# Kernel optimization log

Hardware: AMD Instinct MI355X
Metric: run time of the kernel (lower is better)

The kernel has to match this reference:

```python
import jax, jax.numpy as jnp
import numpy as np

N_SEG, N_REG, N_EDGE, HID, CHEB_K = 40000, 1000, 640000, 256, 5


def setup_inputs() -> dict:
    key = jax.random.key(0)
    ks = jax.random.split(key, 6)
    return {
        "projected_region_features": jax.random.normal(ks[0], (N_REG, HID), jnp.float32),
        "segment2region_assignment": jax.random.uniform(ks[1], (N_SEG, N_REG), jnp.float32),
        "edge_index": jax.random.randint(ks[2], (2, N_EDGE), 0, N_SEG, dtype=jnp.int64),
        # ChebConv params: one [HID,HID] weight per Chebyshev order + shared bias
        "cheb_W": jax.random.normal(ks[3], (CHEB_K, HID, HID), jnp.float32) / np.sqrt(HID).astype(np.float32),
        "cheb_b": jnp.zeros((HID,), jnp.float32),
        "ln_gamma": jnp.ones((HID,), jnp.float32),
        "ln_beta": jnp.zeros((HID,), jnp.float32),
    }


def _cheb_conv(x, edge_index, W, b):
    """PyG ChebConv with normalization='sym', lambda_max=2.0.
    Scaled Laplacian L_hat = 2L/lam - I = -D^{-1/2} A D^{-1/2} (diag = 0)."""
    N = x.shape[0]
    src, dst = edge_index[0], edge_index[1]
    w = (src != dst).astype(x.dtype)  # remove_self_loops
    deg = jax.ops.segment_sum(w, src, num_segments=N)
    dinv = jnp.where(deg > 0, jax.lax.rsqrt(jnp.where(deg > 0, deg, 1.0)), 0.0)
    norm = -w * dinv[src] * dinv[dst]  # per-edge weight of L_hat

    def prop(t):  # y_i = sum_{(j->i)} norm_e * t_j
        return jax.ops.segment_sum(norm[:, None] * t[src], dst, num_segments=N)

    Tx0 = x
    out = Tx0 @ W[0]
    Tx1 = prop(Tx0)
    out = out + Tx1 @ W[1]
    for k in range(2, W.shape[0]):
        Tx2 = 2.0 * prop(Tx1) - Tx0
        out = out + Tx2 @ W[k]
        Tx0, Tx1 = Tx1, Tx2
    return out + b


def _layer_norm(x, g, b, eps=1e-5):
    mu = jnp.mean(x, axis=-1, keepdims=True)
    var = jnp.mean(jnp.square(x - mu), axis=-1, keepdims=True)
    return (x - mu) * jax.lax.rsqrt(var + eps) * g + b


def reference(projected_region_features, segment2region_assignment, edge_index,
              cheb_W, cheb_b, ln_gamma, ln_beta):
    # [n_seg, n_reg] @ [n_reg, hid] -> [n_seg, hid]
    seg_low_raw = segment2region_assignment @ projected_region_features
    seg_low = _cheb_conv(seg_low_raw, edge_index, cheb_W, cheb_b)
    seg_low = _layer_norm(jax.nn.gelu(seg_low, approximate=False), ln_gamma, ln_beta)
    return (seg_low, seg_low_raw)
```

## Files before the change

kernel.cpp:

```cpp
#include <hip/hip_runtime.h>

#define NSEG 40000
#define NREG 1000
#define NEDGE 640000
#define HID 256
#define KCAT 1280
#define LPAD 40
#define NBLK 157

typedef float f32x4 __attribute__((ext_vector_type(4)));
typedef short s16x8 __attribute__((ext_vector_type(8)));
typedef unsigned short u16x4 __attribute__((ext_vector_type(4)));
typedef unsigned short u16x8 __attribute__((ext_vector_type(8)));

__device__ __forceinline__ unsigned short f2bf(float f) {
    unsigned u = __builtin_bit_cast(unsigned, f);
    u += 0x7FFFu + ((u >> 16) & 1u);
    return (unsigned short)(u >> 16);
}
__device__ __forceinline__ float bf2f(unsigned short h) {
    unsigned u = ((unsigned)h) << 16;
    return __builtin_bit_cast(float, u);
}

__global__ void detect_kernel(const unsigned int* __restrict__ E, int* flag) {
    int lane = threadIdx.x;
    unsigned v = E[2 * lane + 1];
    unsigned long long m = __ballot(v == 0u);
    if (lane == 0) *flag = (__popcll(m) >= 48) ? 1 : 0;
}

__device__ __forceinline__ int edge_at(const void* E, int idx, int is64) {
    return is64 ? (int)((const long long*)E)[idx] : ((const int*)E)[idx];
}

__global__ __launch_bounds__(256) void deg_cnt_kernel(const void* __restrict__ E,
                                                      const int* __restrict__ flag,
                                                      int* deg, int* cnt) {
    int e = blockIdx.x * 256 + threadIdx.x;
    if (e >= NEDGE) return;
    int is64 = *flag;
    int s = edge_at(E, e, is64);
    int d = edge_at(E, e + NEDGE, is64);
    if (s != d) {
        atomicAdd(&deg[s], 1);
        atomicAdd(&cnt[d], 1);
    }
}

__global__ __launch_bounds__(256) void dinv_kernel(const int* __restrict__ deg,
                                                   float* __restrict__ dinv) {
    int i = blockIdx.x * 256 + threadIdx.x;
    if (i < NSEG) {
        int d = deg[i];
        dinv[i] = d > 0 ? rsqrtf((float)d) : 0.f;
    }
}

__global__ __launch_bounds__(256) void scan1_kernel(const int* __restrict__ cnt,
                                                    int* __restrict__ bsum) {
    __shared__ int sh[256];
    int t = threadIdx.x;
    int i = blockIdx.x * 256 + t;
    sh[t] = (i < NSEG) ? cnt[i] : 0;
    __syncthreads();
    for (int o = 128; o > 0; o >>= 1) {
        if (t < o) sh[t] += sh[t + o];
        __syncthreads();
    }
    if (t == 0) bsum[blockIdx.x] = sh[0];
}

__global__ __launch_bounds__(256) void scan2_kernel(const int* __restrict__ bsum,
                                                    int* __restrict__ boff,
                                                    int* __restrict__ rowptr) {
    __shared__ int sh[256];
    int t = threadIdx.x;
    int v = (t < NBLK) ? bsum[t] : 0;
    sh[t] = v;
    __syncthreads();
    for (int o = 1; o < 256; o <<= 1) {
        int x = 0;
        if (t >= o) x = sh[t - o];
        __syncthreads();
        if (t >= o) sh[t] += x;
        __syncthreads();
    }
    if (t < NBLK) boff[t] = sh[t] - v;
    if (t == 255) rowptr[NSEG] = sh[255];
}

__global__ __launch_bounds__(256) void scan3_kernel(const int* __restrict__ cnt,
                                                    const int* __restrict__ boff,
                                                    int* __restrict__ rowptr,
                                                    int* __restrict__ cursor) {
    __shared__ int sh[256];
    int t = threadIdx.x;
    int i = blockIdx.x * 256 + t;
    int v = (i < NSEG) ? cnt[i] : 0;
    sh[t] = v;
    __syncthreads();
    for (int o = 1; o < 256; o <<= 1) {
        int x = 0;
        if (t >= o) x = sh[t - o];
        __syncthreads();
        if (t >= o) sh[t] += x;
        __syncthreads();
    }
    if (i < NSEG) {
        int p = boff[blockIdx.x] + sh[t] - v;
        rowptr[i] = p;
        cursor[i] = p;
    }
}

__global__ __launch_bounds__(256) void scatter_kernel(const void* __restrict__ E,
                                                      const int* __restrict__ flag,
                                                      const float* __restrict__ dinv,
                                                      int* cursor,
                                                      int* __restrict__ colidx,
                                                      float* __restrict__ val) {
    int e = blockIdx.x * 256 + threadIdx.x;
    if (e >= NEDGE) return;
    int is64 = *flag;
    int s = edge_at(E, e, is64);
    int d = edge_at(E, e + NEDGE, is64);
    if (s != d) {
        int pos = atomicAdd(&cursor[d], 1);
        colidx[pos] = s;
        val[pos] = -dinv[s] * dinv[d];
    }
}

__global__ void prep_pt_kernel(const float* __restrict__ P, unsigned short* __restrict__ Pt) {
    int n = blockIdx.x;
    for (int k = threadIdx.x; k < NREG; k += blockDim.x)
        Pt[(size_t)n * NREG + k] = f2bf(P[(size_t)k * HID + n]);
}
__global__ void prep_wt_kernel(const float* __restrict__ W, unsigned short* __restrict__ Wt) {
    int n = blockIdx.x;
    for (int k = threadIdx.x; k < KCAT; k += blockDim.x)
        Wt[(size_t)n * KCAT + k] = f2bf(W[(size_t)k * HID + n]);
}

__global__ __launch_bounds__(256) void gemm1_kernel(const float* __restrict__ S,
                                                    const unsigned short* __restrict__ Pt,
                                                    float* __restrict__ raw,
                                                    unsigned short* __restrict__ xcat) {
    __shared__ unsigned short As[64][LPAD];
    __shared__ unsigned short Bs[256][LPAD];
    const int m0 = blockIdx.x * 64;
    const int tid = threadIdx.x;
    const int lane = tid & 63, wn = tid >> 6;
    const int r = lane & 15, q = lane >> 4;
    const int srow = tid >> 2, scol = (tid & 3) * 8;

    f32x4 acc[4][4] = {};

    for (int kb = 0; kb < NREG; kb += 32) {
        const bool kvalid = (kb + scol + 8 <= NREG);
        u16x8 av = {0, 0, 0, 0, 0, 0, 0, 0};
        u16x8 bv0 = av, bv1 = av, bv2 = av, bv3 = av;
        if (kvalid) {
            const float* sp = S + (size_t)(m0 + srow) * NREG + kb + scol;
            f32x4 f0 = *(const f32x4*)sp;
            f32x4 f1 = *(const f32x4*)(sp + 4);
            av[0] = f2bf(f0[0]); av[1] = f2bf(f0[1]); av[2] = f2bf(f0[2]); av[3] = f2bf(f0[3]);
            av[4] = f2bf(f1[0]); av[5] = f2bf(f1[1]); av[6] = f2bf(f1[2]); av[7] = f2bf(f1[3]);
            bv0 = *(const u16x8*)(Pt + (size_t)(srow)       * NREG + kb + scol);
            bv1 = *(const u16x8*)(Pt + (size_t)(srow +  64) * NREG + kb + scol);
            bv2 = *(const u16x8*)(Pt + (size_t)(srow + 128) * NREG + kb + scol);
            bv3 = *(const u16x8*)(Pt + (size_t)(srow + 192) * NREG + kb + scol);
        }
        __syncthreads();
        *(u16x8*)&As[srow][scol] = av;
        *(u16x8*)&Bs[srow][scol] = bv0;
        *(u16x8*)&Bs[srow + 64][scol] = bv1;
        *(u16x8*)&Bs[srow + 128][scol] = bv2;
        *(u16x8*)&Bs[srow + 192][scol] = bv3;
        __syncthreads();
        s16x8 af[4], bfv[4];
#pragma unroll
        for (int am = 0; am < 4; ++am) af[am] = *(const s16x8*)&As[am * 16 + r][q * 8];
#pragma unroll
        for (int bn = 0; bn < 4; ++bn) bfv[bn] = *(const s16x8*)&Bs[wn * 64 + bn * 16 + r][q * 8];
#pragma unroll
        for (int am = 0; am < 4; ++am) {
#pragma unroll
            for (int bn = 0; bn < 4; ++bn)
                acc[am][bn] = __builtin_amdgcn_mfma_f32_16x16x32_bf16(af[am], bfv[bn], acc[am][bn], 0, 0, 0);
        }
    }
#pragma unroll
    for (int am = 0; am < 4; ++am) {
        int rowb = m0 + am * 16 + q * 4;
#pragma unroll
        for (int bn = 0; bn < 4; ++bn) {
            int col = wn * 64 + bn * 16 + r;
#pragma unroll
            for (int i = 0; i < 4; ++i) {
                float v = acc[am][bn][i];
                raw[(size_t)(rowb + i) * HID + col] = v;
                xcat[(size_t)(rowb + i) * KCAT + col] = f2bf(v);
            }
        }
    }
}

__global__ __launch_bounds__(256) void prop_kernel(unsigned short* xcat,
                                                   const int* __restrict__ rowptr,
                                                   const int* __restrict__ colidx,
                                                   const float* __restrict__ val,
                                                   int inOff, int outOff, int subOff,
                                                   float scale) {
    int g = blockIdx.x * 4 + (threadIdx.x >> 6);
    int lane = threadIdx.x & 63;
    int e0 = rowptr[g], e1 = rowptr[g + 1];
    float a0 = 0.f, a1 = 0.f, a2 = 0.f, a3 = 0.f;
    const unsigned short* xin = xcat + inOff + lane * 4;
    for (int base = e0; base < e1; base += 64) {
        int m = e1 - base;
        if (m > 64) m = 64;
        int cc = 0;
        float vv = 0.f;
        if (lane < m) {
            cc = colidx[base + lane];
            vv = val[base + lane];
        }
        int i = 0;
        for (; i + 8 <= m; i += 8) {
            u16x4 t[8];
#pragma unroll
            for (int j = 0; j < 8; ++j) {
                int c = __shfl(cc, i + j);
                t[j] = *(const u16x4*)(xin + (size_t)c * KCAT);
            }
#pragma unroll
            for (int j = 0; j < 8; ++j) {
                float v = __shfl(vv, i + j);
                a0 += v * bf2f(t[j][0]);
                a1 += v * bf2f(t[j][1]);
                a2 += v * bf2f(t[j][2]);
                a3 += v * bf2f(t[j][3]);
            }
        }
        for (; i < m; ++i) {
            int c = __shfl(cc, i);
            float v = __shfl(vv, i);
            u16x4 t = *(const u16x4*)(xin + (size_t)c * KCAT);
            a0 += v * bf2f(t[0]);
            a1 += v * bf2f(t[1]);
            a2 += v * bf2f(t[2]);
            a3 += v * bf2f(t[3]);
        }
    }
    a0 *= scale; a1 *= scale; a2 *= scale; a3 *= scale;
    if (subOff >= 0) {
        u16x4 p = *(const u16x4*)(xcat + (size_t)g * KCAT + subOff + lane * 4);
        a0 -= bf2f(p[0]); a1 -= bf2f(p[1]); a2 -= bf2f(p[2]); a3 -= bf2f(p[3]);
    }
    u16x4 o = {f2bf(a0), f2bf(a1), f2bf(a2), f2bf(a3)};
    *(u16x4*)(xcat + (size_t)g * KCAT + outOff + lane * 4) = o;
}

__global__ __launch_bounds__(256) void gemm2_kernel(const unsigned short* __restrict__ xcat,
                                                    const unsigned short* __restrict__ Wt,
                                                    const float* __restrict__ bias,
                                                    const float* __restrict__ gamma,
                                                    const float* __restrict__ beta,
                                                    float* __restrict__ outp) {
    __shared__ unsigned short As[64][LPAD];
    __shared__ unsigned short Bs[256][LPAD];
    __shared__ float rs[64][4];
    __shared__ float rss[64][4];
    const int m0 = blockIdx.x * 64;
    const int tid = threadIdx.x;
    const int lane = tid & 63, wn = tid >> 6;
    const int r = lane & 15, q = lane >> 4;
    const int srow = tid >> 2, scol = (tid & 3) * 8;

    f32x4 acc[4][4] = {};

    for (int kb = 0; kb < KCAT; kb += 32) {
        u16x8 av  = *(const u16x8*)(xcat + (size_t)(m0 + srow) * KCAT + kb + scol);
        u16x8 bv0 = *(const u16x8*)(Wt + (size_t)(srow)       * KCAT + kb + scol);
        u16x8 bv1 = *(const u16x8*)(Wt + (size_t)(srow +  64) * KCAT + kb + scol);
        u16x8 bv2 = *(const u16x8*)(Wt + (size_t)(srow + 128) * KCAT + kb + scol);
        u16x8 bv3 = *(const u16x8*)(Wt + (size_t)(srow + 192) * KCAT + kb + scol);
        __syncthreads();
        *(u16x8*)&As[srow][scol] = av;
        *(u16x8*)&Bs[srow][scol] = bv0;
        *(u16x8*)&Bs[srow + 64][scol] = bv1;
        *(u16x8*)&Bs[srow + 128][scol] = bv2;
        *(u16x8*)&Bs[srow + 192][scol] = bv3;
        __syncthreads();
        s16x8 af[4], bfv[4];
#pragma unroll
        for (int am = 0; am < 4; ++am) af[am] = *(const s16x8*)&As[am * 16 + r][q * 8];
#pragma unroll
        for (int bn = 0; bn < 4; ++bn) bfv[bn] = *(const s16x8*)&Bs[wn * 64 + bn * 16 + r][q * 8];
#pragma unroll
        for (int am = 0; am < 4; ++am) {
#pragma unroll
            for (int bn = 0; bn < 4; ++bn)
                acc[am][bn] = __builtin_amdgcn_mfma_f32_16x16x32_bf16(af[am], bfv[bn], acc[am][bn], 0, 0, 0);
        }
    }

    float bc[4], gm[4], bt[4];
#pragma unroll
    for (int bn = 0; bn < 4; ++bn) {
        int col = wn * 64 + bn * 16 + r;
        bc[bn] = bias[col];
        gm[bn] = gamma[col];
        bt[bn] = beta[col];
    }
#pragma unroll
    for (int am = 0; am < 4; ++am) {
#pragma unroll
        for (int i = 0; i < 4; ++i) {
            float s = 0.f, ss = 0.f;
#pragma unroll
            for (int bn = 0; bn < 4; ++bn) {
                float v = acc[am][bn][i] + bc[bn];
                v = 0.5f * v * (1.f + erff(v * 0.70710678118654752f));
                acc[am][bn][i] = v;
                s += v;
                ss += v * v;
            }
#pragma unroll
            for (int msk = 1; msk < 16; msk <<= 1) {
                s += __shfl_xor(s, msk);
                ss += __shfl_xor(ss, msk);
            }
            if (r == 0) {
                int row = am * 16 + q * 4 + i;
                rs[row][wn] = s;
                rss[row][wn] = ss;
            }
        }
    }
    __syncthreads();
#pragma unroll
    for (int am = 0; am < 4; ++am) {
#pragma unroll
        for (int i = 0; i < 4; ++i) {
            int row = am * 16 + q * 4 + i;
            float s = rs[row][0] + rs[row][1] + rs[row][2] + rs[row][3];
            float ss = rss[row][0] + rss[row][1] + rss[row][2] + rss[row][3];
            float mu = s * (1.f / HID);
            float var = ss * (1.f / HID) - mu * mu;
            float inv = rsqrtf(var + 1e-5f);
#pragma unroll
            for (int bn = 0; bn < 4; ++bn) {
                int col = wn * 64 + bn * 16 + r;
                outp[(size_t)(m0 + row) * HID + col] = (acc[am][bn][i] - mu) * inv * gm[bn] + bt[bn];
            }
        }
    }
}

extern "C" void kernel_launch(void* const* d_in, const int* in_sizes, int n_in,
                              void* d_out, int out_size, void* d_ws, size_t ws_size,
                              hipStream_t stream) {
    const float* P     = (const float*)d_in[0];
    const float* S     = (const float*)d_in[1];
    const void*  E     = d_in[2];
    const float* W     = (const float*)d_in[3];
    const float* bias  = (const float*)d_in[4];
    const float* gamma = (const float*)d_in[5];
    const float* beta  = (const float*)d_in[6];

    float* out = (float*)d_out;
    float* raw = out + (size_t)NSEG * HID;

    char* ws = (char*)d_ws;
    size_t off = 0;
    auto alloc = [&](size_t bytes) -> void* {
        void* p = ws + off;
        off += (bytes + 255) & ~(size_t)255;
        return p;
    };
    unsigned short* xcat   = (unsigned short*)alloc((size_t)NSEG * KCAT * 2);
    unsigned short* Pt     = (unsigned short*)alloc((size_t)HID * NREG * 2);
    unsigned short* Wt     = (unsigned short*)alloc((size_t)HID * KCAT * 2);
    int*            deg    = (int*)alloc((size_t)NSEG * 4);
    float*          dinv   = (float*)alloc((size_t)NSEG * 4);
    int*            cnt    = (int*)alloc((size_t)NSEG * 4);
    int*            rowptr = (int*)alloc((size_t)(NSEG + 1) * 4);
    int*            cursor = (int*)alloc((size_t)NSEG * 4);
    int*            colidx = (int*)alloc((size_t)NEDGE * 4);
    float*          val    = (float*)alloc((size_t)NEDGE * 4);
    int*            bsum   = (int*)alloc((size_t)NBLK * 4);
    int*            boff   = (int*)alloc((size_t)NBLK * 4);
    int*            flag   = (int*)alloc(256);
    if (off > ws_size) return;

    hipMemsetAsync(deg, 0, (size_t)NSEG * 4, stream);
    hipMemsetAsync(cnt, 0, (size_t)NSEG * 4, stream);

    detect_kernel<<<1, 64, 0, stream>>>((const unsigned int*)E, flag);
    prep_pt_kernel<<<HID, 256, 0, stream>>>(P, Pt);
    prep_wt_kernel<<<HID, 256, 0, stream>>>(W, Wt);

    deg_cnt_kernel<<<NEDGE / 256, 256, 0, stream>>>(E, flag, deg, cnt);
    dinv_kernel<<<(NSEG + 255) / 256, 256, 0, stream>>>(deg, dinv);
    scan1_kernel<<<NBLK, 256, 0, stream>>>(cnt, bsum);
    scan2_kernel<<<1, 256, 0, stream>>>(bsum, boff, rowptr);
    scan3_kernel<<<NBLK, 256, 0, stream>>>(cnt, boff, rowptr, cursor);
    scatter_kernel<<<NEDGE / 256, 256, 0, stream>>>(E, flag, dinv, cursor, colidx, val);

    gemm1_kernel<<<NSEG / 64, 256, 0, stream>>>(S, Pt, raw, xcat);

    prop_kernel<<<NSEG / 4, 256, 0, stream>>>(xcat, rowptr, colidx, val, 0 * HID, 1 * HID, -1, 1.f);
    prop_kernel<<<NSEG / 4, 256, 0, stream>>>(xcat, rowptr, colidx, val, 1 * HID, 2 * HID, 0 * HID, 2.f);
    prop_kernel<<<NSEG / 4, 256, 0, stream>>>(xcat, rowptr, colidx, val, 2 * HID, 3 * HID, 1 * HID, 2.f);
    prop_kernel<<<NSEG / 4, 256, 0, stream>>>(xcat, rowptr, colidx, val, 3 * HID, 4 * HID, 2 * HID, 2.f);

    gemm2_kernel<<<NSEG / 64, 256, 0, stream>>>(xcat, Wt, bias, gamma, beta, out);
}
```

Before: 469.7 us.

## Double-buffer GEMMs with direct global-to-LDS loads and 512-thread blocks

Both GEMM kernels are rewritten to double-buffer LDS tiles, using global_load_lds DMA for the bf16 operands with an XOR-swizzled layout in place of padded rows. Blocks grow to 8 waves laid out as a 2x4 grid, so each wave holds fewer accumulators. Pt is padded to K=1024 with zeros so the tail tile needs no bounds check. The aim is to overlap memory fetch with MFMA work and drop one barrier per k-step. The cost is more LDS per block and tighter coupling to the swizzle and DMA lane mapping.

New measurement: 445.1 us. 5.2% less time.

```diff
diff --git a/kernel.cpp b/kernel.cpp
--- a/kernel.cpp
+++ b/kernel.cpp
@@ -5,7 +5,7 @@
 #define NEDGE 640000
 #define HID 256
 #define KCAT 1280
-#define LPAD 40
+#define KP1 1024
 #define NBLK 157
 
 typedef float f32x4 __attribute__((ext_vector_type(4)));
@@ -13,6 +13,13 @@
 typedef unsigned short u16x4 __attribute__((ext_vector_type(4)));
 typedef unsigned short u16x8 __attribute__((ext_vector_type(8)));
 
+typedef __attribute__((address_space(3))) unsigned int lds_u32;
+typedef __attribute__((address_space(1))) const unsigned int glb_u32;
+
+__device__ __forceinline__ void dma16(const void* g, void* l) {
+    __builtin_amdgcn_global_load_lds((glb_u32*)g, (lds_u32*)l, 16, 0, 0);
+}
+
 __device__ __forceinline__ unsigned short f2bf(float f) {
     unsigned u = __builtin_bit_cast(unsigned, f);
     u += 0x7FFFu + ((u >> 16) & 1u);
@@ -21,6 +28,10 @@
 __device__ __forceinline__ float bf2f(unsigned short h) {
     unsigned u = ((unsigned)h) << 16;
     return __builtin_bit_cast(float, u);
+}
+
+__device__ __forceinline__ f32x4 mfma16(s16x8 a, s16x8 b, f32x4 c) {
+    return __builtin_amdgcn_mfma_f32_16x16x32_bf16(a, b, c, 0, 0, 0);
 }
 
 __global__ void detect_kernel(const unsigned int* __restrict__ E, int* flag) {
@@ -134,8 +145,8 @@
 
 __global__ void prep_pt_kernel(const float* __restrict__ P, unsigned short* __restrict__ Pt) {
     int n = blockIdx.x;
-    for (int k = threadIdx.x; k < NREG; k += blockDim.x)
-        Pt[(size_t)n * NREG + k] = f2bf(P[(size_t)k * HID + n]);
+    for (int k = threadIdx.x; k < KP1; k += blockDim.x)
+        Pt[(size_t)n * KP1 + k] = (k < NREG) ? f2bf(P[(size_t)k * HID + n]) : (unsigned short)0;
 }
 __global__ void prep_wt_kernel(const float* __restrict__ W, unsigned short* __restrict__ Wt) {
     int n = blockIdx.x;
@@ -143,57 +154,70 @@
         Wt[(size_t)n * KCAT + k] = f2bf(W[(size_t)k * HID + n]);
 }
 
-__global__ __launch_bounds__(256) void gemm1_kernel(const float* __restrict__ S,
+__global__ __launch_bounds__(512) void gemm1_kernel(const float* __restrict__ S,
                                                     const unsigned short* __restrict__ Pt,
                                                     float* __restrict__ raw,
                                                     unsigned short* __restrict__ xcat) {
-    __shared__ unsigned short As[64][LPAD];
-    __shared__ unsigned short Bs[256][LPAD];
+    __shared__ unsigned short Af[2][64][40];
+    __shared__ unsigned short Bs[2][256 * 32];
+    const int tid = threadIdx.x;
+    const int lane = tid & 63, wid = tid >> 6;
+    const int wm = wid >> 2, wn = wid & 3;
+    const int r = lane & 15, q = lane >> 4;
+    const int qx = q ^ (r & 3);
     const int m0 = blockIdx.x * 64;
-    const int tid = threadIdx.x;
-    const int lane = tid & 63, wn = tid >> 6;
-    const int r = lane & 15, q = lane >> 4;
-    const int srow = tid >> 2, scol = (tid & 3) * 8;
-
-    f32x4 acc[4][4] = {};
-
-    for (int kb = 0; kb < NREG; kb += 32) {
-        const bool kvalid = (kb + scol + 8 <= NREG);
-        u16x8 av = {0, 0, 0, 0, 0, 0, 0, 0};
-        u16x8 bv0 = av, bv1 = av, bv2 = av, bv3 = av;
-        if (kvalid) {
-            const float* sp = S + (size_t)(m0 + srow) * NREG + kb + scol;
-            f32x4 f0 = *(const f32x4*)sp;
-            f32x4 f1 = *(const f32x4*)(sp + 4);
-            av[0] = f2bf(f0[0]); av[1] = f2bf(f0[1]); av[2] = f2bf(f0[2]); av[3] = f2bf(f0[3]);
-            av[4] = f2bf(f1[0]); av[5] = f2bf(f1[1]); av[6] = f2bf(f1[2]); av[7] = f2bf(f1[3]);
-            bv0 = *(const u16x8*)(Pt + (size_t)(srow)       * NREG + kb + scol);
-            bv1 = *(const u16x8*)(Pt + (size_t)(srow +  64) * NREG + kb + scol);
-            bv2 = *(const u16x8*)(Pt + (size_t)(srow + 128) * NREG + kb + scol);
-            bv3 = *(const u16x8*)(Pt + (size_t)(srow + 192) * NREG + kb + scol);
-        }
-        __syncthreads();
-        *(u16x8*)&As[srow][scol] = av;
-        *(u16x8*)&Bs[srow][scol] = bv0;
-        *(u16x8*)&Bs[srow + 64][scol] = bv1;
-        *(u16x8*)&Bs[srow + 128][scol] = bv2;
-        *(u16x8*)&Bs[srow + 192][scol] = bv3;
-        __syncthreads();
-        s16x8 af[4], bfv[4];
-#pragma unroll
-        for (int am = 0; am < 4; ++am) af[am] = *(const s16x8*)&As[am * 16 + r][q * 8];
-#pragma unroll
-        for (int bn = 0; bn < 4; ++bn) bfv[bn] = *(const s16x8*)&Bs[wn * 64 + bn * 16 + r][q * 8];
-#pragma unroll
-        for (int am = 0; am < 4; ++am) {
+    const int arow = tid >> 3, acol = (tid & 7) * 4;
+    const int j0 = 2 * wid, j1 = j0 + 1;
+    const int brow0 = j0 * 16 + (lane >> 2), brow1 = j1 * 16 + (lane >> 2);
+    const int bcol = (((lane & 3) ^ ((lane >> 2) & 3)) << 3);
+
+    f32x4 acc[2][4] = {};
+    const float* aptr = S + (size_t)(m0 + arow) * NREG;
+
+    auto stageB = [&](int c, int kb) {
+        dma16(Pt + (size_t)brow0 * KP1 + kb + bcol, &Bs[c][j0 * 512]);
+        dma16(Pt + (size_t)brow1 * KP1 + kb + bcol, &Bs[c][j1 * 512]);
+    };
+    auto loadA = [&](int kb) -> f32x4 {
+        int k0 = kb + acol;
+        if (k0 + 4 > NREG) k0 = 0;
+        return *(const f32x4*)(aptr + k0);
+    };
+    auto writeA = [&](int c, f32x4 a) {
+        u16x4 o = {f2bf(a[0]), f2bf(a[1]), f2bf(a[2]), f2bf(a[3])};
+        *(u16x4*)&Af[c][arow][acol] = o;
+    };
+
+    stageB(0, 0);
+    writeA(0, loadA(0));
+    __syncthreads();
+
+    for (int t = 0; t < 32; ++t) {
+        const int c = t & 1;
+        f32x4 an;
+        if (t < 31) {
+            stageB(c ^ 1, (t + 1) * 32);
+            an = loadA((t + 1) * 32);
+        }
+        s16x8 af[2], bf[4];
+#pragma unroll
+        for (int am = 0; am < 2; ++am)
+            af[am] = *(const s16x8*)&Af[c][wm * 32 + am * 16 + r][q * 8];
+#pragma unroll
+        for (int bn = 0; bn < 4; ++bn)
+            bf[bn] = *(const s16x8*)&Bs[c][(wn * 64 + bn * 16 + r) * 32 + qx * 8];
+#pragma unroll
+        for (int am = 0; am < 2; ++am)
 #pragma unroll
             for (int bn = 0; bn < 4; ++bn)
-                acc[am][bn] = __builtin_amdgcn_mfma_f32_16x16x32_bf16(af[am], bfv[bn], acc[am][bn], 0, 0, 0);
-        }
-    }
-#pragma unroll
-    for (int am = 0; am < 4; ++am) {
-        int rowb = m0 + am * 16 + q * 4;
+                acc[am][bn] = mfma16(af[am], bf[bn], acc[am][bn]);
+        if (t < 31) writeA(c ^ 1, an);
+        __syncthreads();
+    }
+
+#pragma unroll
+    for (int am = 0; am < 2; ++am) {
+        int rowb = m0 + wm * 32 + am * 16 + q * 4;
 #pragma unroll
         for (int bn = 0; bn < 4; ++bn) {
             int col = wn * 64 + bn * 16 + r;
@@ -263,48 +287,55 @@
     *(u16x4*)(xcat + (size_t)g * KCAT + outOff + lane * 4) = o;
 }
 
-__global__ __launch_bounds__(256) void gemm2_kernel(const unsigned short* __restrict__ xcat,
+__global__ __launch_bounds__(512) void gemm2_kernel(const unsigned short* __restrict__ xcat,
                                                     const unsigned short* __restrict__ Wt,
                                                     const float* __restrict__ bias,
                                                     const float* __restrict__ gamma,
                                                     const float* __restrict__ beta,
                                                     float* __restrict__ outp) {
-    __shared__ unsigned short As[64][LPAD];
-    __shared__ unsigned short Bs[256][LPAD];
+    __shared__ unsigned short Af[2][64 * 32];
+    __shared__ unsigned short Bs[2][256 * 32];
     __shared__ float rs[64][4];
     __shared__ float rss[64][4];
+    const int tid = threadIdx.x;
+    const int lane = tid & 63, wid = tid >> 6;
+    const int wm = wid >> 2, wn = wid & 3;
+    const int r = lane & 15, q = lane >> 4;
+    const int qx = q ^ (r & 3);
     const int m0 = blockIdx.x * 64;
-    const int tid = threadIdx.x;
-    const int lane = tid & 63, wn = tid >> 6;
-    const int r = lane & 15, q = lane >> 4;
-    const int srow = tid >> 2, scol = (tid & 3) * 8;
-
-    f32x4 acc[4][4] = {};
-
-    for (int kb = 0; kb < KCAT; kb += 32) {
-        u16x8 av  = *(const u16x8*)(xcat + (size_t)(m0 + srow) * KCAT + kb + scol);
-        u16x8 bv0 = *(const u16x8*)(Wt + (size_t)(srow)       * KCAT + kb + scol);
-        u16x8 bv1 = *(const u16x8*)(Wt + (size_t)(srow +  64) * KCAT + kb + scol);
-        u16x8 bv2 = *(const u16x8*)(Wt + (size_t)(srow + 128) * KCAT + kb + scol);
-        u16x8 bv3 = *(const u16x8*)(Wt + (size_t)(srow + 192) * KCAT + kb + scol);
-        __syncthreads();
-        *(u16x8*)&As[srow][scol] = av;
-        *(u16x8*)&Bs[srow][scol] = bv0;
-        *(u16x8*)&Bs[srow + 64][scol] = bv1;
-        *(u16x8*)&Bs[srow + 128][scol] = bv2;
-        *(u16x8*)&Bs[srow + 192][scol] = bv3;
-        __syncthreads();
-        s16x8 af[4], bfv[4];
-#pragma unroll
-        for (int am = 0; am < 4; ++am) af[am] = *(const s16x8*)&As[am * 16 + r][q * 8];
-#pragma unroll
-        for (int bn = 0; bn < 4; ++bn) bfv[bn] = *(const s16x8*)&Bs[wn * 64 + bn * 16 + r][q * 8];
-#pragma unroll
-        for (int am = 0; am < 4; ++am) {
+    const int j0 = 2 * wid, j1 = j0 + 1;
+    const int brow0 = j0 * 16 + (lane >> 2), brow1 = j1 * 16 + (lane >> 2);
+    const int arowd = wid * 16 + (lane >> 2);
+    const int bcol = (((lane & 3) ^ ((lane >> 2) & 3)) << 3);
+
+    f32x4 acc[2][4] = {};
+
+    auto stage = [&](int c, int kb) {
+        dma16(Wt + (size_t)brow0 * KCAT + kb + bcol, &Bs[c][j0 * 512]);
+        dma16(Wt + (size_t)brow1 * KCAT + kb + bcol, &Bs[c][j1 * 512]);
+        if (wid < 4)
+            dma16(xcat + (size_t)(m0 + arowd) * KCAT + kb + bcol, &Af[c][wid * 512]);
+    };
+
+    stage(0, 0);
+    __syncthreads();
+
+    for (int t = 0; t < 40; ++t) {
+        const int c = t & 1;
+        if (t < 39) stage(c ^ 1, (t + 1) * 32);
+        s16x8 af[2], bf[4];
+#pragma unroll
+        for (int am = 0; am < 2; ++am)
+            af[am] = *(const s16x8*)&Af[c][(wm * 32 + am * 16 + r) * 32 + qx * 8];
+#pragma unroll
+        for (int bn = 0; bn < 4; ++bn)
+            bf[bn] = *(const s16x8*)&Bs[c][(wn * 64 + bn * 16 + r) * 32 + qx * 8];
+#pragma unroll
+        for (int am = 0; am < 2; ++am)
 #pragma unroll
             for (int bn = 0; bn < 4; ++bn)
-                acc[am][bn] = __builtin_amdgcn_mfma_f32_16x16x32_bf16(af[am], bfv[bn], acc[am][bn], 0, 0, 0);
-        }
+                acc[am][bn] = mfma16(af[am], bf[bn], acc[am][bn]);
+        __syncthreads();
     }
 
     float bc[4], gm[4], bt[4];
@@ -316,7 +347,7 @@
         bt[bn] = beta[col];
     }
 #pragma unroll
-    for (int am = 0; am < 4; ++am) {
+    for (int am = 0; am < 2; ++am) {
 #pragma unroll
         for (int i = 0; i < 4; ++i) {
             float s = 0.f, ss = 0.f;
@@ -334,7 +365,7 @@
                 ss += __shfl_xor(ss, msk);
             }
             if (r == 0) {
-                int row = am * 16 + q * 4 + i;
+                int row = wm * 32 + am * 16 + q * 4 + i;
                 rs[row][wn] = s;
                 rss[row][wn] = ss;
             }
@@ -342,10 +373,10 @@
     }
     __syncthreads();
 #pragma unroll
-    for (int am = 0; am < 4; ++am) {
+    for (int am = 0; am < 2; ++am) {
 #pragma unroll
         for (int i = 0; i < 4; ++i) {
-            int row = am * 16 + q * 4 + i;
+            int row = wm * 32 + am * 16 + q * 4 + i;
             float s = rs[row][0] + rs[row][1] + rs[row][2] + rs[row][3];
             float ss = rss[row][0] + rss[row][1] + rss[row][2] + rss[row][3];
             float mu = s * (1.f / HID);
@@ -382,7 +413,7 @@
         return p;
     };
     unsigned short* xcat   = (unsigned short*)alloc((size_t)NSEG * KCAT * 2);
-    unsigned short* Pt     = (unsigned short*)alloc((size_t)HID * NREG * 2);
+    unsigned short* Pt     = (unsigned short*)alloc((size_t)HID * KP1 * 2);
     unsigned short* Wt     = (unsigned short*)alloc((size_t)HID * KCAT * 2);
     int*            deg    = (int*)alloc((size_t)NSEG * 4);
     float*          dinv   = (float*)alloc((size_t)NSEG * 4);
@@ -410,12 +441,12 @@
     scan3_kernel<<<NBLK, 256, 0, stream>>>(cnt, boff, rowptr, cursor);
     scatter_kernel<<<NEDGE / 256, 256, 0, stream>>>(E, flag, dinv, cursor, colidx, val);
 
-    gemm1_kernel<<<NSEG / 64, 256, 0, stream>>>(S, Pt, raw, xcat);
+    gemm1_kernel<<<NSEG / 64, 512, 0, stream>>>(S, Pt, raw, xcat);
 
     prop_kernel<<<NSEG / 4, 256, 0, stream>>>(xcat, rowptr, colidx, val, 0 * HID, 1 * HID, -1, 1.f);
     prop_kernel<<<NSEG / 4, 256, 0, stream>>>(xcat, rowptr, colidx, val, 1 * HID, 2 * HID, 0 * HID, 2.f);
     prop_kernel<<<NSEG / 4, 256, 0, stream>>>(xcat, rowptr, colidx, val, 2 * HID, 3 * HID, 1 * HID, 2.f);
     prop_kernel<<<NSEG / 4, 256, 0, stream>>>(xcat, rowptr, colidx, val, 3 * HID, 4 * HID, 2 * HID, 2.f);
 
-    gemm2_kernel<<<NSEG / 64, 256, 0, stream>>>(xcat, Wt, bias, gamma, beta, out);
-}
+    gemm2_kernel<<<NSEG / 64, 512, 0, stream>>>(xcat, Wt, bias, gamma, beta, out);
+}
```

## Pipeline GEMM K-loops with direct global-to-LDS loads and swizzled shared tiles

Applied to the files above, without the earlier changes.

Both GEMM kernels now use a 4-slot B ring buffer filled with global_load_lds DMA, a double-buffered A tile with register prefetch several stages ahead, and XOR-swizzled LDS layouts in place of padding. The goal is to overlap global memory latency with MFMA work and to drop one of the two barriers per K step. Pt is padded to K=1024 so the DMA loads need no bounds checks. The hand-written vmcnt waits and unrolled prologue and epilogue are fragile: a wrong count causes a race, and the extra LDS may reduce occupancy.

New measurement: 468.0 us. Within noise of the previous version (-0.4%).

```diff
diff --git a/kernel.cpp b/kernel.cpp
--- a/kernel.cpp
+++ b/kernel.cpp
@@ -5,7 +5,7 @@
 #define NEDGE 640000
 #define HID 256
 #define KCAT 1280
-#define LPAD 40
+#define KP1 1024
 #define NBLK 157
 
 typedef float f32x4 __attribute__((ext_vector_type(4)));
@@ -13,6 +13,13 @@
 typedef unsigned short u16x4 __attribute__((ext_vector_type(4)));
 typedef unsigned short u16x8 __attribute__((ext_vector_type(8)));
 
+typedef __attribute__((address_space(3))) unsigned int lds_u32;
+typedef __attribute__((address_space(1))) const unsigned int glb_u32;
+
+__device__ __forceinline__ void dma16(const void* g, void* l) {
+    __builtin_amdgcn_global_load_lds((glb_u32*)g, (lds_u32*)l, 16, 0, 0);
+}
+
 __device__ __forceinline__ unsigned short f2bf(float f) {
     unsigned u = __builtin_bit_cast(unsigned, f);
     u += 0x7FFFu + ((u >> 16) & 1u);
@@ -22,6 +29,16 @@
     unsigned u = ((unsigned)h) << 16;
     return __builtin_bit_cast(float, u);
 }
+
+__device__ __forceinline__ f32x4 mfma16(s16x8 a, s16x8 b, f32x4 c) {
+    return __builtin_amdgcn_mfma_f32_16x16x32_bf16(a, b, c, 0, 0, 0);
+}
+
+#define FENCE(VMN)                                                   \
+    asm volatile("s_waitcnt vmcnt(" #VMN ")" ::: "memory");          \
+    asm volatile("s_waitcnt lgkmcnt(0)" ::: "memory");               \
+    __builtin_amdgcn_s_barrier();                                    \
+    __builtin_amdgcn_sched_barrier(0);
 
 __global__ void detect_kernel(const unsigned int* __restrict__ E, int* flag) {
     int lane = threadIdx.x;
@@ -134,8 +151,8 @@
 
 __global__ void prep_pt_kernel(const float* __restrict__ P, unsigned short* __restrict__ Pt) {
     int n = blockIdx.x;
-    for (int k = threadIdx.x; k < NREG; k += blockDim.x)
-        Pt[(size_t)n * NREG + k] = f2bf(P[(size_t)k * HID + n]);
+    for (int k = threadIdx.x; k < KP1; k += blockDim.x)
+        Pt[(size_t)n * KP1 + k] = (k < NREG) ? f2bf(P[(size_t)k * HID + n]) : (unsigned short)0;
 }
 __global__ void prep_wt_kernel(const float* __restrict__ W, unsigned short* __restrict__ Wt) {
     int n = blockIdx.x;
@@ -147,50 +164,92 @@
                                                     const unsigned short* __restrict__ Pt,
                                                     float* __restrict__ raw,
                                                     unsigned short* __restrict__ xcat) {
-    __shared__ unsigned short As[64][LPAD];
-    __shared__ unsigned short Bs[256][LPAD];
-    const int m0 = blockIdx.x * 64;
+    __shared__ unsigned short As[2][64 * 32];
+    __shared__ unsigned short Bs[4][256 * 32];
     const int tid = threadIdx.x;
     const int lane = tid & 63, wn = tid >> 6;
     const int r = lane & 15, q = lane >> 4;
-    const int srow = tid >> 2, scol = (tid & 3) * 8;
+    const int qx8 = (q ^ (r & 3)) << 3;
+    const int m0 = blockIdx.x * 64;
+    const int arow = tid >> 2, acol = (tid & 3) * 8;
+    const int ag = (((acol >> 3) ^ (arow & 3)) << 3);
+    const int crow = lane >> 2;
+    const int bcol = (((lane & 3) ^ (crow & 3)) << 3);
+    const float* aptr = S + (size_t)(m0 + arow) * NREG;
 
     f32x4 acc[4][4] = {};
-
-    for (int kb = 0; kb < NREG; kb += 32) {
-        const bool kvalid = (kb + scol + 8 <= NREG);
-        u16x8 av = {0, 0, 0, 0, 0, 0, 0, 0};
-        u16x8 bv0 = av, bv1 = av, bv2 = av, bv3 = av;
-        if (kvalid) {
-            const float* sp = S + (size_t)(m0 + srow) * NREG + kb + scol;
-            f32x4 f0 = *(const f32x4*)sp;
-            f32x4 f1 = *(const f32x4*)(sp + 4);
-            av[0] = f2bf(f0[0]); av[1] = f2bf(f0[1]); av[2] = f2bf(f0[2]); av[3] = f2bf(f0[3]);
-            av[4] = f2bf(f1[0]); av[5] = f2bf(f1[1]); av[6] = f2bf(f1[2]); av[7] = f2bf(f1[3]);
-            bv0 = *(const u16x8*)(Pt + (size_t)(srow)       * NREG + kb + scol);
-            bv1 = *(const u16x8*)(Pt + (size_t)(srow +  64) * NREG + kb + scol);
-            bv2 = *(const u16x8*)(Pt + (size_t)(srow + 128) * NREG + kb + scol);
-            bv3 = *(const u16x8*)(Pt + (size_t)(srow + 192) * NREG + kb + scol);
-        }
-        __syncthreads();
-        *(u16x8*)&As[srow][scol] = av;
-        *(u16x8*)&Bs[srow][scol] = bv0;
-        *(u16x8*)&Bs[srow + 64][scol] = bv1;
-        *(u16x8*)&Bs[srow + 128][scol] = bv2;
-        *(u16x8*)&Bs[srow + 192][scol] = bv3;
-        __syncthreads();
+    f32x4 rl0, rh0, rl1, rh1, rl2, rh2, rl3, rh3;
+
+    auto stageB = [&](int slot, int kb) {
+#pragma unroll
+        for (int k = 0; k < 4; ++k) {
+            int j = wn * 4 + k;
+            dma16(Pt + (size_t)(j * 16 + crow) * KP1 + kb + bcol, &Bs[slot][j * 512]);
+        }
+    };
+    auto loadA = [&](int kb, f32x4& lo, f32x4& hi) {
+        int k0 = kb + acol;
+        if (k0 + 8 > NREG) k0 = 0;
+        lo = *(const f32x4*)(aptr + k0);
+        hi = *(const f32x4*)(aptr + k0 + 4);
+    };
+    auto convA = [&](int par, const f32x4& lo, const f32x4& hi) {
+        u16x8 o = {f2bf(lo[0]), f2bf(lo[1]), f2bf(lo[2]), f2bf(lo[3]),
+                   f2bf(hi[0]), f2bf(hi[1]), f2bf(hi[2]), f2bf(hi[3])};
+        *(u16x8*)&As[par][arow * 32 + ag] = o;
+    };
+    auto compute = [&](int slot, int par) {
         s16x8 af[4], bfv[4];
 #pragma unroll
-        for (int am = 0; am < 4; ++am) af[am] = *(const s16x8*)&As[am * 16 + r][q * 8];
-#pragma unroll
-        for (int bn = 0; bn < 4; ++bn) bfv[bn] = *(const s16x8*)&Bs[wn * 64 + bn * 16 + r][q * 8];
-#pragma unroll
-        for (int am = 0; am < 4; ++am) {
+        for (int am = 0; am < 4; ++am)
+            af[am] = *(const s16x8*)&As[par][(am * 16 + r) * 32 + qx8];
+#pragma unroll
+        for (int bn = 0; bn < 4; ++bn)
+            bfv[bn] = *(const s16x8*)&Bs[slot][(wn * 64 + bn * 16 + r) * 32 + qx8];
+#pragma unroll
+        for (int am = 0; am < 4; ++am)
 #pragma unroll
             for (int bn = 0; bn < 4; ++bn)
-                acc[am][bn] = __builtin_amdgcn_mfma_f32_16x16x32_bf16(af[am], bfv[bn], acc[am][bn], 0, 0, 0);
-        }
-    }
+                acc[am][bn] = mfma16(af[am], bfv[bn], acc[am][bn]);
+    };
+
+    loadA(0, rl0, rh0);
+    stageB(0, 0);  loadA(32, rl1, rh1);
+    stageB(1, 32); loadA(64, rl2, rh2);
+    stageB(2, 64); loadA(96, rl3, rh3);
+    asm volatile("s_waitcnt vmcnt(12)" ::: "memory");
+    convA(0, rl0, rh0);
+    asm volatile("s_waitcnt lgkmcnt(0)" ::: "memory");
+    __builtin_amdgcn_s_barrier();
+    __builtin_amdgcn_sched_barrier(0);
+
+#define G1_STEP(J, TT, RLL, RHL, RLC, RHC, VMN)   \
+    stageB(((J) + 3) & 3, ((TT) + 3) * 32);       \
+    loadA(((TT) + 4) * 32, RLL, RHL);             \
+    convA(((TT) + 1) & 1, RLC, RHC);              \
+    compute((J), (TT) & 1);                       \
+    FENCE(VMN)
+
+    for (int u = 0; u < 7; ++u) {
+        const int t = u * 4;
+        G1_STEP(0, t + 0, rl0, rh0, rl1, rh1, 12);
+        G1_STEP(1, t + 1, rl1, rh1, rl2, rh2, 12);
+        G1_STEP(2, t + 2, rl2, rh2, rl3, rh3, 12);
+        G1_STEP(3, t + 3, rl3, rh3, rl0, rh0, 12);
+    }
+#undef G1_STEP
+    stageB(3, 992);
+    convA(1, rl1, rh1);
+    compute(0, 0);
+    FENCE(10)
+    convA(0, rl2, rh2);
+    compute(1, 1);
+    FENCE(4)
+    convA(1, rl3, rh3);
+    compute(2, 0);
+    FENCE(0)
+    compute(3, 1);
+
 #pragma unroll
     for (int am = 0; am < 4; ++am) {
         int rowb = m0 + am * 16 + q * 4;
@@ -269,43 +328,88 @@
                                                     const float* __restrict__ gamma,
                                                     const float* __restrict__ beta,
                                                     float* __restrict__ outp) {
-    __shared__ unsigned short As[64][LPAD];
-    __shared__ unsigned short Bs[256][LPAD];
+    __shared__ unsigned short As[2][64 * 32];
+    __shared__ unsigned short Bs[4][256 * 32];
     __shared__ float rs[64][4];
     __shared__ float rss[64][4];
-    const int m0 = blockIdx.x * 64;
     const int tid = threadIdx.x;
     const int lane = tid & 63, wn = tid >> 6;
     const int r = lane & 15, q = lane >> 4;
-    const int srow = tid >> 2, scol = (tid & 3) * 8;
+    const int qx8 = (q ^ (r & 3)) << 3;
+    const int m0 = blockIdx.x * 64;
+    const int arow = tid >> 2, acol = (tid & 3) * 8;
+    const int ag = (((acol >> 3) ^ (arow & 3)) << 3);
+    const int crow = lane >> 2;
+    const int bcol = (((lane & 3) ^ (crow & 3)) << 3);
+    const unsigned short* aptr = xcat + (size_t)(m0 + arow) * KCAT;
 
     f32x4 acc[4][4] = {};
-
-    for (int kb = 0; kb < KCAT; kb += 32) {
-        u16x8 av  = *(const u16x8*)(xcat + (size_t)(m0 + srow) * KCAT + kb + scol);
-        u16x8 bv0 = *(const u16x8*)(Wt + (size_t)(srow)       * KCAT + kb + scol);
-        u16x8 bv1 = *(const u16x8*)(Wt + (size_t)(srow +  64) * KCAT + kb + scol);
-        u16x8 bv2 = *(const u16x8*)(Wt + (size_t)(srow + 128) * KCAT + kb + scol);
-        u16x8 bv3 = *(const u16x8*)(Wt + (size_t)(srow + 192) * KCAT + kb + scol);
-        __syncthreads();
-        *(u16x8*)&As[srow][scol] = av;
-        *(u16x8*)&Bs[srow][scol] = bv0;
-        *(u16x8*)&Bs[srow + 64][scol] = bv1;
-        *(u16x8*)&Bs[srow + 128][scol] = bv2;
-        *(u16x8*)&Bs[srow + 192][scol] = bv3;
-        __syncthreads();
+    u16x8 ra0, ra1, ra2, ra3;
+
+    auto stageB = [&](int slot, int kb) {
+#pragma unroll
+        for (int k = 0; k < 4; ++k) {
+            int j = wn * 4 + k;
+            dma16(Wt + (size_t)(j * 16 + crow) * KCAT + kb + bcol, &Bs[slot][j * 512]);
+        }
+    };
+    auto loadA = [&](int kb, u16x8& a) {
+        a = *(const u16x8*)(aptr + kb + acol);
+    };
+    auto convA = [&](int par, const u16x8& a) {
+        *(u16x8*)&As[par][arow * 32 + ag] = a;
+    };
+    auto compute = [&](int slot, int par) {
         s16x8 af[4], bfv[4];
 #pragma unroll
-        for (int am = 0; am < 4; ++am) af[am] = *(const s16x8*)&As[am * 16 + r][q * 8];
-#pragma unroll
-        for (int bn = 0; bn < 4; ++bn) bfv[bn] = *(const s16x8*)&Bs[wn * 64 + bn * 16 + r][q * 8];
-#pragma unroll
-        for (int am = 0; am < 4; ++am) {
+        for (int am = 0; am < 4; ++am)
+            af[am] = *(const s16x8*)&As[par][(am * 16 + r) * 32 + qx8];
+#pragma unroll
+        for (int bn = 0; bn < 4; ++bn)
+            bfv[bn] = *(const s16x8*)&Bs[slot][(wn * 64 + bn * 16 + r) * 32 + qx8];
+#pragma unroll
+        for (int am = 0; am < 4; ++am)
 #pragma unroll
             for (int bn = 0; bn < 4; ++bn)
-                acc[am][bn] = __builtin_amdgcn_mfma_f32_16x16x32_bf16(af[am], bfv[bn], acc[am][bn], 0, 0, 0);
-        }
-    }
+                acc[am][bn] = mfma16(af[am], bfv[bn], acc[am][bn]);
+    };
+
+    loadA(0, ra0);
+    stageB(0, 0);  loadA(32, ra1);
+    stageB(1, 32); loadA(64, ra2);
+    stageB(2, 64); loadA(96, ra3);
+    asm volatile("s_waitcnt vmcnt(10)" ::: "memory");
+    convA(0, ra0);
+    asm volatile("s_waitcnt lgkmcnt(0)" ::: "memory");
+    __builtin_amdgcn_s_barrier();
+    __builtin_amdgcn_sched_barrier(0);
+
+#define G2_STEP(J, TT, RAL, RAC, VMN)             \
+    stageB(((J) + 3) & 3, ((TT) + 3) * 32);       \
+    loadA(((TT) + 4) * 32, RAL);                  \
+    convA(((TT) + 1) & 1, RAC);                   \
+    compute((J), (TT) & 1);                       \
+    FENCE(VMN)
+
+    for (int u = 0; u < 9; ++u) {
+        const int t = u * 4;
+        G2_STEP(0, t + 0, ra0, ra1, 10);
+        G2_STEP(1, t + 1, ra1, ra2, 10);
+        G2_STEP(2, t + 2, ra2, ra3, 10);
+        G2_STEP(3, t + 3, ra3, ra0, 10);
+    }
+#undef G2_STEP
+    stageB(3, 39 * 32);
+    convA(1, ra1);
+    compute(0, 0);
+    FENCE(9)
+    convA(0, ra2);
+    compute(1, 1);
+    FENCE(4)
+    convA(1, ra3);
+    compute(2, 0);
+    FENCE(0)
+    compute(3, 1);
 
     float bc[4], gm[4], bt[4];
 #pragma unroll
@@ -382,7 +486,7 @@
         return p;
     };
     unsigned short* xcat   = (unsigned short*)alloc((size_t)NSEG * KCAT * 2);
-    unsigned short* Pt     = (unsigned short*)alloc((size_t)HID * NREG * 2);
+    unsigned short* Pt     = (unsigned short*)alloc((size_t)HID * KP1 * 2);
     unsigned short* Wt     = (unsigned short*)alloc((size_t)HID * KCAT * 2);
     int*            deg    = (int*)alloc((size_t)NSEG * 4);
     float*          dinv   = (float*)alloc((size_t)NSEG * 4);
```
